# Kernel tuning notes

Measured on AMD Instinct MI355X. Metric: run time of the kernel, lower is better.

Reference implementation:

```python
import jax, jax.numpy as jnp
import numpy as np

BLOCK_M = 64
BLOCK_N = 64
CAUSAL = True


def setup_inputs() -> dict:
    key = jax.random.key(0)
    kq, kk, kv, km = jax.random.split(key, 4)
    B, T, H, Dqk, Dv = 2, 2048, 16, 128, 128
    q = jax.random.normal(kq, (B, T, H, Dqk), dtype=jnp.float16)
    k = jax.random.normal(kk, (B, T, H, Dqk), dtype=jnp.float16)
    v = jax.random.normal(kv, (B, T, H, Dv), dtype=jnp.float16)
    nq = T // BLOCK_M  # 32 query blocks
    nk = T // BLOCK_N  # 32 kv blocks
    block_mask = jax.random.randint(km, (B, H, nq, nk), 0, 2).astype(bool)
    # force diagonal blocks on so every (causal) query row has >=1 valid key
    eye = jnp.eye(nq, nk, dtype=bool)
    block_mask = block_mask | eye[None, None, :, :]
    return {"q": q, "k": k, "v": v, "block_mask": block_mask}


def reference(q, k, v, block_mask):
    B, T, H, Dqk = q.shape
    Dv = v.shape[-1]
    scale = 1.0 / np.sqrt(Dqk).astype(np.float32)
    qf = q.astype(jnp.float32)
    kf = k.astype(jnp.float32)
    vf = v.astype(jnp.float32)
    # groups == 1: k/v already have H heads
    scores = jnp.einsum('bthd,bshd->bhts', qf, kf) * scale  # [B,H,T,T]
    # expand block mask [B,H,nq,nk] -> [B,H,T,T]
    mask = jnp.repeat(jnp.repeat(block_mask, BLOCK_M, axis=2), BLOCK_N, axis=3)
    if CAUSAL:
        causal = jnp.tril(jnp.ones((T, T), dtype=bool))
        mask = mask & causal[None, None, :, :]
    scores = jnp.where(mask, scores, -jnp.inf)
    weights = jax.nn.softmax(scores, axis=-1)
    out = jnp.einsum('bhts,bshd->bthd', weights, vf)
    return out.astype(jnp.float16)
```

## Files before the change

kernel.cpp:

```cpp
#include <hip/hip_runtime.h>


typedef _Float16 half8 __attribute__((ext_vector_type(8)));
typedef float floatx16 __attribute__((ext_vector_type(16)));

#define B_ 2
#define T_ 2048
#define H_ 16
#define D_ 128
#define BM 64
#define BN 64
#define NQ (T_ / BM)
#define NK (T_ / BN)
#define PSTR 40
#define TILE_HALVES 8192

#define GLOAD_LDS16(g, l) \
    __builtin_amdgcn_global_load_lds((const __attribute__((address_space(1))) void*)(g), \
                                     (__attribute__((address_space(3))) void*)(l), 16, 0, 0)

__device__ inline half8 cvt8(const float4 a, const float4 b) {
    half8 r;
    r[0] = (_Float16)a.x; r[1] = (_Float16)a.y;
    r[2] = (_Float16)a.z; r[3] = (_Float16)a.w;
    r[4] = (_Float16)b.x; r[5] = (_Float16)b.y;
    r[6] = (_Float16)b.z; r[7] = (_Float16)b.w;
    return r;
}

__device__ inline int vswz(int d) {
    return (((d & 7) ^ ((d >> 3) & 7)) << 3);
}

__global__ __launch_bounds__(256)
void cast_kv_kernel(const float* __restrict__ kg, const float* __restrict__ vg,
                    _Float16* __restrict__ wsk, _Float16* __restrict__ wsv)
{
    const int tile = blockIdx.x;
    const int pair = tile >> 5;
    const int j    = tile & 31;
    const int b    = pair >> 4;
    const int h    = pair & 15;
    const int tid  = threadIdx.x;

    const size_t rowstr = H_ * D_;
    const size_t base = ((size_t)b * T_ + (size_t)j * BN) * rowstr + (size_t)h * D_;
    _Float16* imk = wsk + (size_t)tile * TILE_HALVES;
    _Float16* imv = wsv + (size_t)tile * TILE_HALVES;

    #pragma unroll
    for (int kk = 0; kk < 4; ++kk) {
        const int c  = tid + 256 * kk;
        const int s  = c >> 4;
        const int d8 = (c & 15) << 3;
        const float* kp = kg + base + (size_t)s * rowstr + d8;
        float4 a  = *(const float4*)kp;
        float4 bb = *(const float4*)(kp + 4);
        *(half8*)(&imk[s * 128 + (d8 ^ ((s & 7) << 3))]) = cvt8(a, bb);
    }
    const int vd  = (tid & 63) * 2;
    const int vsg = tid >> 6;
    #pragma unroll
    for (int p = 0; p < 2; ++p) {
        half8 r0, r1;
        #pragma unroll
        for (int i = 0; i < 8; ++i) {
            const float* vp = vg + base + (size_t)(vsg * 16 + p * 8 + i) * rowstr + vd;
            float2 vv = *(const float2*)vp;
            r0[i] = (_Float16)vv.x;
            r1[i] = (_Float16)vv.y;
        }
        const int sb = vsg * 16 + p * 8;
        *(half8*)(&imv[vd * 64 + (sb ^ vswz(vd))])           = r0;
        *(half8*)(&imv[(vd + 1) * 64 + (sb ^ vswz(vd + 1))]) = r1;
    }
}

__global__ __launch_bounds__(256, 2)
void bsattn_kernel(const float* __restrict__ qg,
                   const _Float16* __restrict__ wsk,
                   const _Float16* __restrict__ wsv,
                   const int* __restrict__ maskg,
                   float* __restrict__ outg)
{
    const int m0   = blockIdx.x;
    const int xcd  = m0 & 7;
    const int slot = m0 >> 3;
    const int pair = xcd * 4 + (slot >> 4);
    const int t    = slot & 15;
    const int b    = pair >> 4;
    const int h    = pair & 15;

    const int tid  = threadIdx.x;
    const int wave = tid >> 6;
    const int wr   = wave >> 1;
    const int wc   = wave & 1;
    const int lane = tid & 63;
    const int l31  = lane & 31;
    const int hi   = lane >> 5;

    __shared__ _Float16 smem[2 * 16384 + 4 * 32 * PSTR];
    _Float16* Pw = smem + 2 * 16384 + wave * (32 * PSTR);

    const float cs2 = 0.08838834764831845f * 1.44269504088896341f;
    const float C2  = 6.0f * 1.44269504088896341f;

    const size_t tilebase = (size_t)pair * NK * TILE_HALVES;

    half8 ones8;
    #pragma unroll
    for (int e = 0; e < 8; ++e) ones8[e] = (_Float16)1.0f;

    auto stage = [&](int j, int bet) {
        const _Float16* imk = wsk + tilebase + (size_t)j * TILE_HALVES;
        const _Float16* imv = wsv + tilebase + (size_t)j * TILE_HALVES;
        _Float16* Kb = smem + bet * 16384;
        _Float16* Vb = Kb + 8192;
        #pragma unroll
        for (int i = 0; i < 4; ++i) {
            const int off = wave * 2048 + i * 512;
            GLOAD_LDS16(imk + off + lane * 8, Kb + off);
            GLOAD_LDS16(imv + off + lane * 8, Vb + off);
        }
    };

    half8 qf[8];
    auto loadQ = [&](int qi) {
        const int qrow = qi * BM + wr * 32 + l31;
        const float* qp = qg + (((size_t)b * T_ + qrow) * H_ + h) * D_;
        #pragma unroll
        for (int kc = 0; kc < 8; ++kc) {
            float4 a = *(const float4*)(qp + kc * 16 + hi * 8);
            float4 c = *(const float4*)(qp + kc * 16 + hi * 8 + 4);
            qf[kc] = cvt8(a, c);
        }
    };

    const int qiA = 31 - t, qiB = t;
    const int* mbase = maskg + (((size_t)b * H_ + h) * NQ) * NK;
    unsigned actA = 0, actB = 0;
    #pragma unroll
    for (int j = 0; j < NK; ++j) {
        const int mA = mbase[qiA * NK + j];
        const int mB = mbase[qiB * NK + j];
        actA |= ((j <= qiA) && mA) ? (1u << j) : 0u;
        actB |= ((j <= qiB) && mB) ? (1u << j) : 0u;
    }

    int beta = 0;
    loadQ(qiA);
    int jcur = __ffs(actA) - 1;
    unsigned rem = actA & (actA - 1);
    stage(jcur, 0);

    #pragma unroll 1
    for (int seg = 0; seg < 2; ++seg) {
        const int qi = seg ? qiB : qiA;

        floatx16 acc[4];
        #pragma unroll
        for (int u = 0; u < 4; ++u) acc[u] = (floatx16)0.0f;
        floatx16 lacc0 = (floatx16)0.0f;
        floatx16 lacc1 = (floatx16)0.0f;

        while (true) {
            __syncthreads();

            int jnext = -1;
            if (rem) {
                jnext = __ffs(rem) - 1;
                rem &= rem - 1;
                stage(jnext, beta ^ 1);
            } else if (seg == 0) {
                stage(__ffs(actB) - 1, beta ^ 1);
            }

            const _Float16* Kb = smem + beta * 16384;
            const _Float16* Vb = Kb + 8192;
            const bool diag = (jcur == qi);

            if (!(diag && wc > wr)) {
                floatx16 s0 = (floatx16)0.0f, s1 = (floatx16)0.0f;
                {
                    const _Float16* Krow = Kb + (32 * wc + l31) * 128;
                    const int ksw = (l31 & 7) << 3;
                    #pragma unroll
                    for (int kc = 0; kc < 4; ++kc) {
                        half8 kf = *(const half8*)(Krow + ((kc * 16 + hi * 8) ^ ksw));
                        s0 = __builtin_amdgcn_mfma_f32_32x32x16_f16(qf[kc], kf, s0, 0, 0, 0);
                    }
                    #pragma unroll
                    for (int kc = 4; kc < 8; ++kc) {
                        half8 kf = *(const half8*)(Krow + ((kc * 16 + hi * 8) ^ ksw));
                        s1 = __builtin_amdgcn_mfma_f32_32x32x16_f16(qf[kc], kf, s1, 0, 0, 0);
                    }
                }
                floatx16 sacc = s0 + s1;

                if (diag && wc == wr) {
                    #pragma unroll
                    for (int r = 0; r < 16; ++r) {
                        const int rq = (r & 3) + 8 * (r >> 2) + 4 * hi;
                        if (l31 > rq) sacc[r] = -INFINITY;
                    }
                }

                #pragma unroll
                for (int r = 0; r < 16; ++r) {
                    const int rq = (r & 3) + 8 * (r >> 2) + 4 * hi;
                    const float p = __builtin_amdgcn_exp2f(__builtin_fmaf(sacc[r], cs2, -C2));
                    Pw[rq * PSTR + l31] = (_Float16)p;
                }

                half8 pf[2];
                #pragma unroll
                for (int kvc = 0; kvc < 2; ++kvc)
                    pf[kvc] = *(const half8*)(&Pw[l31 * PSTR + kvc * 16 + hi * 8]);

                lacc0 = __builtin_amdgcn_mfma_f32_32x32x16_f16(ones8, pf[0], lacc0, 0, 0, 0);
                lacc1 = __builtin_amdgcn_mfma_f32_32x32x16_f16(ones8, pf[1], lacc1, 0, 0, 0);

                #pragma unroll
                for (int dt = 0; dt < 4; ++dt) {
                    const int d  = dt * 32 + l31;
                    const int sw = vswz(d);
                    const _Float16* Vrow = Vb + d * 64;
                    #pragma unroll
                    for (int kvc = 0; kvc < 2; ++kvc) {
                        half8 vf = *(const half8*)(Vrow + ((32 * wc + kvc * 16 + hi * 8) ^ sw));
                        acc[dt] = __builtin_amdgcn_mfma_f32_32x32x16_f16(vf, pf[kvc], acc[dt], 0, 0, 0);
                    }
                }
            }

            if (jnext < 0) break;
            jcur = jnext;
            beta ^= 1;
        }

        if (seg == 0) loadQ(qiB);

        __syncthreads();
        float* Ebuf = (float*)(smem + beta * 16384);
        float* Lbuf = (float*)(smem + 2 * 16384);

        #pragma unroll
        for (int dt = 0; dt < 4; ++dt) {
            if ((dt >> 1) != wc) {
                const int tt = dt & 1;
                #pragma unroll
                for (int g = 0; g < 4; ++g) {
                    float4 val;
                    val.x = acc[dt][4 * g + 0];
                    val.y = acc[dt][4 * g + 1];
                    val.z = acc[dt][4 * g + 2];
                    val.w = acc[dt][4 * g + 3];
                    const int idx = (((((wr * 2 + wc) * 2 + tt) * 4 + g) * 2 + hi) * 32 + l31);
                    *(float4*)(&Ebuf[idx * 4]) = val;
                }
            }
        }
        const float lmine = lacc0[0] + lacc1[0];
        Lbuf[(wr * 2 + wc) * 32 + l31] = lmine;
        __syncthreads();

        const float ltot = lmine + Lbuf[(wr * 2 + (1 - wc)) * 32 + l31];
        const float inv  = 1.0f / ltot;
        const int qrow   = qi * BM + wr * 32 + l31;
        float* op = outg + (((size_t)b * T_ + qrow) * H_ + h) * D_;

        #pragma unroll
        for (int dt = 0; dt < 4; ++dt) {
            if ((dt >> 1) == wc) {
                const int tt = dt & 1;
                #pragma unroll
                for (int g = 0; g < 4; ++g) {
                    const int idx = (((((wr * 2 + (1 - wc)) * 2 + tt) * 4 + g) * 2 + hi) * 32 + l31);
                    float4 p = *(const float4*)(&Ebuf[idx * 4]);
                    float4 o;
                    o.x = (acc[dt][4 * g + 0] + p.x) * inv;
                    o.y = (acc[dt][4 * g + 1] + p.y) * inv;
                    o.z = (acc[dt][4 * g + 2] + p.z) * inv;
                    o.w = (acc[dt][4 * g + 3] + p.w) * inv;
                    *(float4*)(op + dt * 32 + g * 8 + hi * 4) = o;
                }
            }
        }

        if (seg == 0) {
            beta ^= 1;
            jcur = __ffs(actB) - 1;
            rem  = actB & (actB - 1);
        }
    }
}

extern "C" void kernel_launch(void* const* d_in, const int* in_sizes, int n_in,
                              void* d_out, int out_size, void* d_ws, size_t ws_size,
                              hipStream_t stream) {
    const float* q  = (const float*)d_in[0];
    const float* k  = (const float*)d_in[1];
    const float* v  = (const float*)d_in[2];
    const int* mask = (const int*)d_in[3];
    float* out      = (float*)d_out;

    _Float16* wsk = (_Float16*)d_ws;
    _Float16* wsv = wsk + (size_t)B_ * H_ * NK * TILE_HALVES;

    cast_kv_kernel<<<dim3(B_ * H_ * NK), 256, 0, stream>>>(k, v, wsk, wsv);
    bsattn_kernel<<<dim3(512), 256, 0, stream>>>(q, wsk, wsv, mask, out);
}
```

Before: 171.8 us.

## Replace static paired query-block scheduling with atomic work-queue persistent blocks

The cast kernel now precomputes per-(query block, head) active-KV bitmasks with a ballot and resets a global counter. The attention kernel drops the fixed pairing of query blocks t and 31-t and instead grabs work items dynamically through an atomic counter, ordered from the longest query rows first. It prefetches the next item's first K/V tile while the current item finishes, so loads overlap across items. This is meant to balance the uneven per-block work that the random block mask creates. In exchange it adds atomics, extra barriers, and the loss of the previous XCD-aware placement, which may reduce L2 reuse.

```diff
diff --git a/kernel.cpp b/kernel.cpp
--- a/kernel.cpp
+++ b/kernel.cpp
@@ -12,6 +12,7 @@
 #define BN 64
 #define NQ (T_ / BM)
 #define NK (T_ / BN)
+#define NITEMS (B_ * H_ * NQ)
 #define PSTR 40
 #define TILE_HALVES 8192
 
@@ -34,7 +35,9 @@
 
 __global__ __launch_bounds__(256)
 void cast_kv_kernel(const float* __restrict__ kg, const float* __restrict__ vg,
-                    _Float16* __restrict__ wsk, _Float16* __restrict__ wsv)
+                    const int* __restrict__ maskg,
+                    _Float16* __restrict__ wsk, _Float16* __restrict__ wsv,
+                    int* __restrict__ ws_act, int* __restrict__ ws_ctr)
 {
     const int tile = blockIdx.x;
     const int pair = tile >> 5;
@@ -74,23 +77,25 @@
         *(half8*)(&imv[vd * 64 + (sb ^ vswz(vd))])           = r0;
         *(half8*)(&imv[(vd + 1) * 64 + (sb ^ vswz(vd + 1))]) = r1;
     }
+
+    if (tid < 64) {
+        int pred = 0;
+        if (tid < 32 && tid <= j)
+            pred = (maskg[(((size_t)b * H_ + h) * NQ + j) * NK + tid] != 0);
+        unsigned long long bal = __ballot(pred);
+        if (tid == 0) ws_act[(31 - j) * 32 + pair] = (int)(unsigned)bal;
+    }
+    if (tile == 0 && tid == 0) *ws_ctr = 0;
 }
 
 __global__ __launch_bounds__(256, 2)
 void bsattn_kernel(const float* __restrict__ qg,
                    const _Float16* __restrict__ wsk,
                    const _Float16* __restrict__ wsv,
-                   const int* __restrict__ maskg,
+                   const int* __restrict__ ws_act,
+                   int* __restrict__ ws_ctr,
                    float* __restrict__ outg)
 {
-    const int m0   = blockIdx.x;
-    const int xcd  = m0 & 7;
-    const int slot = m0 >> 3;
-    const int pair = xcd * 4 + (slot >> 4);
-    const int t    = slot & 15;
-    const int b    = pair >> 4;
-    const int h    = pair & 15;
-
     const int tid  = threadIdx.x;
     const int wave = tid >> 6;
     const int wr   = wave >> 1;
@@ -100,20 +105,19 @@
     const int hi   = lane >> 5;
 
     __shared__ _Float16 smem[2 * 16384 + 4 * 32 * PSTR];
+    __shared__ int sh_next;
     _Float16* Pw = smem + 2 * 16384 + wave * (32 * PSTR);
 
     const float cs2 = 0.08838834764831845f * 1.44269504088896341f;
     const float C2  = 6.0f * 1.44269504088896341f;
-
-    const size_t tilebase = (size_t)pair * NK * TILE_HALVES;
 
     half8 ones8;
     #pragma unroll
     for (int e = 0; e < 8; ++e) ones8[e] = (_Float16)1.0f;
 
-    auto stage = [&](int j, int bet) {
-        const _Float16* imk = wsk + tilebase + (size_t)j * TILE_HALVES;
-        const _Float16* imv = wsv + tilebase + (size_t)j * TILE_HALVES;
+    auto stage = [&](size_t tb, int j, int bet) {
+        const _Float16* imk = wsk + tb + (size_t)j * TILE_HALVES;
+        const _Float16* imv = wsv + tb + (size_t)j * TILE_HALVES;
         _Float16* Kb = smem + bet * 16384;
         _Float16* Vb = Kb + 8192;
         #pragma unroll
@@ -125,9 +129,9 @@
     };
 
     half8 qf[8];
-    auto loadQ = [&](int qi) {
-        const int qrow = qi * BM + wr * 32 + l31;
-        const float* qp = qg + (((size_t)b * T_ + qrow) * H_ + h) * D_;
+    auto loadQ = [&](int bb, int hh, int qq) {
+        const int qrow = qq * BM + wr * 32 + l31;
+        const float* qp = qg + (((size_t)bb * T_ + qrow) * H_ + hh) * D_;
         #pragma unroll
         for (int kc = 0; kc < 8; ++kc) {
             float4 a = *(const float4*)(qp + kc * 16 + hi * 8);
@@ -136,32 +140,37 @@
         }
     };
 
-    const int qiA = 31 - t, qiB = t;
-    const int* mbase = maskg + (((size_t)b * H_ + h) * NQ) * NK;
-    unsigned actA = 0, actB = 0;
-    #pragma unroll
-    for (int j = 0; j < NK; ++j) {
-        const int mA = mbase[qiA * NK + j];
-        const int mB = mbase[qiB * NK + j];
-        actA |= ((j <= qiA) && mA) ? (1u << j) : 0u;
-        actB |= ((j <= qiB) && mB) ? (1u << j) : 0u;
-    }
-
+    if (tid == 0) sh_next = atomicAdd(ws_ctr, 1);
+    __syncthreads();
+    int item = sh_next;
+    if (item >= NITEMS) return;
+
+    int qi   = 31 - (item >> 5);
+    int pair = item & 31;
+    int b    = pair >> 4;
+    int h    = pair & 15;
+    size_t tilebase = (size_t)pair * NK * TILE_HALVES;
+    unsigned act = (unsigned)ws_act[item];
+    int jcur = __ffs(act) - 1;
+    unsigned rem = act & (act - 1);
     int beta = 0;
-    loadQ(qiA);
-    int jcur = __ffs(actA) - 1;
-    unsigned rem = actA & (actA - 1);
-    stage(jcur, 0);
+    stage(tilebase, jcur, 0);
+    loadQ(b, h, qi);
 
     #pragma unroll 1
-    for (int seg = 0; seg < 2; ++seg) {
-        const int qi = seg ? qiB : qiA;
+    while (true) {
+        bool grab_pending = (rem == 0);
 
         floatx16 acc[4];
         #pragma unroll
         for (int u = 0; u < 4; ++u) acc[u] = (floatx16)0.0f;
         floatx16 lacc0 = (floatx16)0.0f;
         floatx16 lacc1 = (floatx16)0.0f;
+
+        int nit = NITEMS;
+        int nqi = 0, npair = 0;
+        size_t ntb = 0;
+        unsigned nact = 0;
 
         while (true) {
             __syncthreads();
@@ -170,9 +179,21 @@
             if (rem) {
                 jnext = __ffs(rem) - 1;
                 rem &= rem - 1;
-                stage(jnext, beta ^ 1);
-            } else if (seg == 0) {
-                stage(__ffs(actB) - 1, beta ^ 1);
+                if (rem == 0 && tid == 0) sh_next = atomicAdd(ws_ctr, 1);
+                stage(tilebase, jnext, beta ^ 1);
+            } else {
+                if (grab_pending) {
+                    if (tid == 0) sh_next = atomicAdd(ws_ctr, 1);
+                    __syncthreads();
+                }
+                nit = sh_next;
+                if (nit < NITEMS) {
+                    nqi   = 31 - (nit >> 5);
+                    npair = nit & 31;
+                    ntb   = (size_t)npair * NK * TILE_HALVES;
+                    nact  = (unsigned)ws_act[nit];
+                    stage(ntb, __ffs(nact) - 1, beta ^ 1);
+                }
             }
 
             const _Float16* Kb = smem + beta * 16384;
@@ -238,7 +259,7 @@
             beta ^= 1;
         }
 
-        if (seg == 0) loadQ(qiB);
+        if (nit < NITEMS) loadQ(npair >> 4, npair & 15, nqi);
 
         __syncthreads();
         float* Ebuf = (float*)(smem + beta * 16384);
@@ -287,11 +308,17 @@
             }
         }
 
-        if (seg == 0) {
-            beta ^= 1;
-            jcur = __ffs(actB) - 1;
-            rem  = actB & (actB - 1);
-        }
+        if (nit >= NITEMS) return;
+
+        item = nit;
+        qi   = nqi;
+        pair = npair;
+        b    = pair >> 4;
+        h    = pair & 15;
+        tilebase = ntb;
+        jcur = __ffs(nact) - 1;
+        rem  = nact & (nact - 1);
+        beta ^= 1;
     }
 }
 
@@ -306,7 +333,10 @@
 
     _Float16* wsk = (_Float16*)d_ws;
     _Float16* wsv = wsk + (size_t)B_ * H_ * NK * TILE_HALVES;
-
-    cast_kv_kernel<<<dim3(B_ * H_ * NK), 256, 0, stream>>>(k, v, wsk, wsv);
-    bsattn_kernel<<<dim3(512), 256, 0, stream>>>(q, wsk, wsv, mask, out);
-}
+    int* ws_act   = (int*)(wsv + (size_t)B_ * H_ * NK * TILE_HALVES);
+    int* ws_ctr   = ws_act + NITEMS;
+
+    cast_kv_kernel<<<dim3(B_ * H_ * NK), 256, 0, stream>>>(k, v, mask, wsk, wsv,
+                                                           ws_act, ws_ctr);
+    bsattn_kernel<<<dim3(512), 256, 0, stream>>>(q, wsk, wsv, ws_act, ws_ctr, out);
+}
```

Result: slower. 179.7 us (+4.6%).
